# Optimization experiments

Measured on AMD Instinct MI355X. Metric: run time of the kernel, lower is better.

The kernel has to match this reference:

```python
import jax, jax.numpy as jnp
import numpy as np

B, T, V = 8, 1024, 2048

def setup_inputs() -> dict:
    key = jax.random.key(0)
    k1, k2, k3 = jax.random.split(key, 3)
    idx = jax.random.randint(k1, (B, T), 0, V)
    v_weight = jnp.zeros((T, 1), dtype=jnp.float32) + 0.02 * jax.random.normal(k2, (T, 1), dtype=jnp.float32)
    W = 0.01 * jnp.ones((V, V), dtype=jnp.float32) + 0.001 * jax.random.normal(k3, (V, V), dtype=jnp.float32)
    return {"idx": idx, "v_weight": v_weight, "W": W}

def reference(idx, v_weight, W):
    Tn = idx.shape[1]
    Vn = W.shape[0]
    e = jax.nn.one_hot(idx, Vn, dtype=jnp.float32)            # [B,T,V]
    pos = jnp.arange(Tn)
    rel = jnp.maximum(pos[:, None] - pos[None, :], 0)          # [T,T] clamped relative positions
    causal = pos[:, None] >= pos[None, :]                      # True where attention allowed
    # Layer 1: positional attention (shared across batch)
    a1 = v_weight[rel, 0]                                      # [T,T] gather from v embedding
    a1 = jnp.where(causal, a1, -jnp.inf)
    a1 = jax.nn.softmax(a1, axis=-1)
    layer_one = jnp.einsum('ts,bsv->btv', a1, e)               # [B,T,V]
    key_t = layer_one @ W.T                                    # Linear without bias: x @ W^T
    # Layer 2: content attention
    a2 = jnp.einsum('btv,bsv->bts', e, key_t)                  # [B,T,T]
    a2 = jnp.where(causal[None], a2, -jnp.inf)
    a2 = jax.nn.softmax(a2, axis=-1)
    logits = jnp.einsum('bts,bsv->btv', a2, e)                 # [B,T,V]
    return logits
```

## Files before the change

kernel.cpp:

```cpp
#include <hip/hip_runtime.h>
#include <hip/hip_bf16.h>
#include <math.h>

#define Bn 8
#define Tn 1024
#define Vn 2048

typedef __attribute__((ext_vector_type(8))) __bf16 bf16x8;
typedef __attribute__((ext_vector_type(4))) float floatx4;

#define GLDS(gp, lp) \
    __builtin_amdgcn_global_load_lds( \
        (const __attribute__((address_space(1))) void*)(gp), \
        (__attribute__((address_space(3))) void*)(lp), 16, 0, 0)

__global__ __launch_bounds__(256) void k_prep(const int* __restrict__ idx,
                                              const float* __restrict__ W,
                                              const float* __restrict__ vw,
                                              __hip_bfloat16* __restrict__ Abf,
                                              __hip_bfloat16* __restrict__ BT) {
    __shared__ float sbuf[Vn];
    int tid = threadIdx.x;
    if (blockIdx.y == Bn) {
        int s = blockIdx.x;
        int wave = tid >> 6, lane = tid & 63;
        float part = 0.0f;
#pragma unroll
        for (int i = 0; i < 4; ++i) {
            int d = tid + i * 256;
            if (d <= s) part += __expf(vw[d]);
        }
#pragma unroll
        for (int off = 32; off > 0; off >>= 1) part += __shfl_xor(part, off);
        if (lane == 0) sbuf[wave] = part;
        __syncthreads();
        float cinv = 1.0f / (sbuf[0] + sbuf[1] + sbuf[2] + sbuf[3]);
        int k0 = tid * 4;
        ushort u[4];
#pragma unroll
        for (int j = 0; j < 4; ++j) {
            int k = k0 + j;
            float v = (k <= s) ? __expf(vw[s - k]) * cinv : 0.0f;
            __hip_bfloat16 h = __float2bfloat16(v);
            u[j] = *reinterpret_cast<ushort*>(&h);
        }
        *reinterpret_cast<ushort4*>(&BT[(size_t)s * Tn + k0]) =
            make_ushort4(u[0], u[1], u[2], u[3]);
    } else {
        int b = blockIdx.y, t = blockIdx.x;
        int r = idx[b * Tn + t];
        const float* Wr = W + (size_t)r * Vn;
#pragma unroll
        for (int i = 0; i < 2; ++i) {
            int o = (tid + i * 256) * 4;
            *reinterpret_cast<float4*>(&sbuf[o]) = *reinterpret_cast<const float4*>(&Wr[o]);
        }
        int kmax = ((t >> 7) + 1) << 7;
        int k0 = tid * 4;
        int4 c4 = *reinterpret_cast<const int4*>(&idx[b * Tn + k0]);
        __syncthreads();
        if (k0 < kmax) {
            ushort u[4];
            __hip_bfloat16 h;
            h = __float2bfloat16(sbuf[c4.x]); u[0] = *reinterpret_cast<ushort*>(&h);
            h = __float2bfloat16(sbuf[c4.y]); u[1] = *reinterpret_cast<ushort*>(&h);
            h = __float2bfloat16(sbuf[c4.z]); u[2] = *reinterpret_cast<ushort*>(&h);
            h = __float2bfloat16(sbuf[c4.w]); u[3] = *reinterpret_cast<ushort*>(&h);
            *reinterpret_cast<ushort4*>(&Abf[((size_t)(b * Tn + t)) * Tn + k0]) =
                make_ushort4(u[0], u[1], u[2], u[3]);
        }
    }
}

#define TM 128
#define TN 128
#define NCHUNK 46

__device__ const signed char CH_MI[NCHUNK] = {7,7,6,7,5,6,7,4,5,6,7,3,4,5,6,7,
                                              6,7,2,3,4,5,6,7,
                                              5,6,7,1,2,3,4,5,6,7,
                                              4,5,6,7,0,1,2,3,4,5,6,7};
__device__ const signed char CH_NI[NCHUNK] = {7,7,6,6,5,5,5,4,4,4,4,3,3,3,3,3,
                                              6,6,2,2,2,2,2,2,
                                              5,5,5,1,1,1,1,1,1,1,
                                              4,4,4,4,0,0,0,0,0,0,0,0};
__device__ const signed char CH_K0[NCHUNK] = {0,8,0,0,0,0,0,0,0,0,0,0,0,0,0,0,
                                              8,8,0,0,0,0,0,0,
                                              8,8,8,0,0,0,0,0,0,0,
                                              8,8,8,8,0,0,0,0,0,0,0,0};
__device__ const signed char CH_K1[NCHUNK] = {8,16,8,8,8,8,8,8,8,8,8,8,8,8,8,8,
                                              14,14,6,6,6,6,6,6,
                                              12,12,12,4,4,4,4,4,4,4,
                                              10,10,10,10,2,2,2,2,2,2,2,2};
__device__ const signed char CH_P[NCHUNK]  = {0,1,0,0,0,0,0,0,0,0,0,0,0,0,0,0,
                                              1,1,0,0,0,0,0,0,
                                              1,1,1,0,0,0,0,0,0,0,
                                              1,1,1,1,0,0,0,0,0,0,0,0};

__global__ __launch_bounds__(256) void k_gemm(const __hip_bfloat16* __restrict__ A,
                                              const __hip_bfloat16* __restrict__ BT,
                                              float* __restrict__ part0,
                                              float* __restrict__ part1) {
    __shared__ __align__(16) __hip_bfloat16 As[16 * 512];
    __shared__ __align__(16) __hip_bfloat16 Bs[16 * 512];
    int b = blockIdx.x;
    int cidx = blockIdx.y;
    int mi = CH_MI[cidx], ni = CH_NI[cidx];
    int ki0 = CH_K0[cidx], ki1 = CH_K1[cidx];
    int m0 = mi * TM, n0 = ni * TN;
    int tid = threadIdx.x;
    int wave = tid >> 6, lane = tid & 63;
    int lr = lane & 15, lq = lane >> 4;
    int wmsub = (wave >> 1) * 4, wnsub = (wave & 1) * 4;

    const __hip_bfloat16* Ab = A + (size_t)b * Tn * Tn;

    const __hip_bfloat16* aS[4];
    const __hip_bfloat16* bS[4];
    __hip_bfloat16* aD[4];
    __hip_bfloat16* bD[4];
#pragma unroll
    for (int j = 0; j < 4; ++j) {
        int c = wave * 4 + j;
        int sub = c & 7, h = c >> 3;
        aS[j] = Ab + (size_t)(m0 + sub * 16 + lr) * Tn + h * 32 + lq * 8;
        bS[j] = BT + (size_t)(n0 + sub * 16 + lr) * Tn + h * 32 + lq * 8;
        aD[j] = &As[c * 512];
        bD[j] = &Bs[c * 512];
    }

    floatx4 acc[4][4];
#pragma unroll
    for (int i = 0; i < 4; ++i)
#pragma unroll
        for (int j = 0; j < 4; ++j) acc[i][j] = (floatx4){0.f, 0.f, 0.f, 0.f};

    for (int ki = ki0; ki < ki1; ++ki) {
        int ko = ki * 64;
#pragma unroll
        for (int j = 0; j < 4; ++j) {
            GLDS(aS[j] + ko, aD[j]);
            GLDS(bS[j] + ko, bD[j]);
        }
        __syncthreads();
        bf16x8 af[2][4], bfr[2][4];
#pragma unroll
        for (int h = 0; h < 2; ++h) {
#pragma unroll
            for (int m = 0; m < 4; ++m)
                af[h][m] = *reinterpret_cast<const bf16x8*>(
                    &As[(h * 8 + wmsub + m) * 512 + lane * 8]);
#pragma unroll
            for (int n = 0; n < 4; ++n)
                bfr[h][n] = *reinterpret_cast<const bf16x8*>(
                    &Bs[(h * 8 + wnsub + n) * 512 + lane * 8]);
        }
#pragma unroll
        for (int h = 0; h < 2; ++h)
#pragma unroll
            for (int m = 0; m < 4; ++m)
#pragma unroll
                for (int n = 0; n < 4; ++n)
                    acc[m][n] = __builtin_amdgcn_mfma_f32_16x16x32_bf16(
                        af[h][m], bfr[h][n], acc[m][n], 0, 0, 0);
        __syncthreads();
    }

    float* Cb = (CH_P[cidx] ? part1 : part0) + (size_t)b * Tn * Tn;
    int quad = lane >> 4;
#pragma unroll
    for (int m = 0; m < 4; ++m)
#pragma unroll
        for (int n = 0; n < 4; ++n)
#pragma unroll
            for (int r = 0; r < 4; ++r) {
                int row = m0 + wmsub * 16 + m * 16 + quad * 4 + r;
                int col = n0 + wnsub * 16 + n * 16 + lr;
                Cb[(size_t)row * Tn + col] = acc[m][n][r];
            }
}

__global__ __launch_bounds__(256) void k_softscat(const float* __restrict__ part0,
                                                  const float* __restrict__ part1,
                                                  const int* __restrict__ idx,
                                                  float* __restrict__ out) {
    __shared__ float sh[Vn];
    __shared__ float red[4];
    int t = blockIdx.x, b = blockIdx.y, tid = threadIdx.x;
    int wave = tid >> 6, lane = tid & 63;
#pragma unroll
    for (int i = 0; i < Vn / 256; ++i) sh[tid + i * 256] = 0.0f;

    size_t rowoff = ((size_t)b * Tn + t) * Tn;
    int s0 = tid * 4;
    float v[4] = {0.f, 0.f, 0.f, 0.f};
    if (s0 <= t) {
        float4 v4 = *reinterpret_cast<const float4*>(&part0[rowoff + s0]);
        v[0] = v4.x; v[1] = v4.y; v[2] = v4.z; v[3] = v4.w;
        if (s0 >= 512) {
            float4 w4 = *reinterpret_cast<const float4*>(&part1[rowoff + s0]);
            v[0] += w4.x; v[1] += w4.y; v[2] += w4.z; v[3] += w4.w;
        }
    }
    int4 c4 = *reinterpret_cast<const int4*>(&idx[b * Tn + s0]);
    float e[4];
    float lsum = 0.f;
#pragma unroll
    for (int j = 0; j < 4; ++j) {
        e[j] = (s0 + j <= t) ? __expf(v[j]) : 0.0f;
        lsum += e[j];
    }
#pragma unroll
    for (int off = 32; off > 0; off >>= 1) lsum += __shfl_xor(lsum, off);
    if (lane == 0) red[wave] = lsum;
    __syncthreads();
    float inv = 1.0f / (red[0] + red[1] + red[2] + red[3]);
    int c[4] = {c4.x, c4.y, c4.z, c4.w};
#pragma unroll
    for (int j = 0; j < 4; ++j)
        if (s0 + j <= t) atomicAdd(&sh[c[j]], e[j] * inv);
    __syncthreads();
    float* orow = out + ((size_t)b * Tn + t) * Vn;
#pragma unroll
    for (int i = 0; i < Vn / (256 * 4); ++i) {
        floatx4 val = *reinterpret_cast<const floatx4*>(&sh[(tid + i * 256) * 4]);
        __builtin_nontemporal_store(val,
            reinterpret_cast<floatx4*>(&orow[(tid + i * 256) * 4]));
    }
}

extern "C" void kernel_launch(void* const* d_in, const int* in_sizes, int n_in,
                              void* d_out, int out_size, void* d_ws, size_t ws_size,
                              hipStream_t stream) {
    const int* idx = (const int*)d_in[0];
    const float* vw = (const float*)d_in[1];
    const float* W = (const float*)d_in[2];
    float* out = (float*)d_out;
    char* ws = (char*)d_ws;

    __hip_bfloat16* BT = (__hip_bfloat16*)(ws);
    __hip_bfloat16* Abf = (__hip_bfloat16*)(ws + (2u << 20));
    float* part0 = (float*)(ws + (18u << 20));
    float* part1 = (float*)(ws + (52u << 20));

    k_prep<<<dim3(Tn, Bn + 1), 256, 0, stream>>>(idx, W, vw, Abf, BT);
    k_gemm<<<dim3(Bn, NCHUNK), 256, 0, stream>>>(Abf, BT, part0, part1);
    k_softscat<<<dim3(Tn, Bn), 256, 0, stream>>>(part0, part1, idx, out);
}
```

Before: 136.5 us.

## Double-buffer GEMM LDS tiles and stream W rows via global_load_lds

The GEMM main loop now uses two LDS buffers, issuing the next k-tile's direct-to-LDS loads before computing the current tile. Explicit vmcnt waits and raw barriers replace the syncthreads, so global latency can overlap MFMA work. The prep kernel also loads the gathered W row straight into LDS with global_load_lds and skips idx loads for columns past the causal limit. This doubles LDS use per GEMM block, which may reduce occupancy, and depends on hand-written waitcnt values being correct.

```diff
diff --git a/kernel.cpp b/kernel.cpp
--- a/kernel.cpp
+++ b/kernel.cpp
@@ -19,7 +19,7 @@
                                               const float* __restrict__ vw,
                                               __hip_bfloat16* __restrict__ Abf,
                                               __hip_bfloat16* __restrict__ BT) {
-    __shared__ float sbuf[Vn];
+    __shared__ __align__(16) float sbuf[Vn];
     int tid = threadIdx.x;
     if (blockIdx.y == Bn) {
         int s = blockIdx.x;
@@ -48,16 +48,17 @@
             make_ushort4(u[0], u[1], u[2], u[3]);
     } else {
         int b = blockIdx.y, t = blockIdx.x;
+        int wave = tid >> 6;
         int r = idx[b * Tn + t];
         const float* Wr = W + (size_t)r * Vn;
 #pragma unroll
         for (int i = 0; i < 2; ++i) {
-            int o = (tid + i * 256) * 4;
-            *reinterpret_cast<float4*>(&sbuf[o]) = *reinterpret_cast<const float4*>(&Wr[o]);
+            GLDS(Wr + i * 1024 + tid * 4, &sbuf[i * 1024 + wave * 256]);
         }
         int kmax = ((t >> 7) + 1) << 7;
         int k0 = tid * 4;
-        int4 c4 = *reinterpret_cast<const int4*>(&idx[b * Tn + k0]);
+        int4 c4 = make_int4(0, 0, 0, 0);
+        if (k0 < kmax) c4 = *reinterpret_cast<const int4*>(&idx[b * Tn + k0]);
         __syncthreads();
         if (k0 < kmax) {
             ushort u[4];
@@ -75,6 +76,7 @@
 #define TM 128
 #define TN 128
 #define NCHUNK 46
+#define BUFE (16 * 512)
 
 __device__ const signed char CH_MI[NCHUNK] = {7,7,6,7,5,6,7,4,5,6,7,3,4,5,6,7,
                                               6,7,2,3,4,5,6,7,
@@ -101,8 +103,8 @@
                                               const __hip_bfloat16* __restrict__ BT,
                                               float* __restrict__ part0,
                                               float* __restrict__ part1) {
-    __shared__ __align__(16) __hip_bfloat16 As[16 * 512];
-    __shared__ __align__(16) __hip_bfloat16 Bs[16 * 512];
+    __shared__ __align__(16) __hip_bfloat16 As[2 * BUFE];
+    __shared__ __align__(16) __hip_bfloat16 Bs[2 * BUFE];
     int b = blockIdx.x;
     int cidx = blockIdx.y;
     int mi = CH_MI[cidx], ni = CH_NI[cidx];
@@ -135,25 +137,42 @@
 #pragma unroll
         for (int j = 0; j < 4; ++j) acc[i][j] = (floatx4){0.f, 0.f, 0.f, 0.f};
 
+#pragma unroll
+    for (int j = 0; j < 4; ++j) {
+        GLDS(aS[j] + ki0 * 64, aD[j]);
+        GLDS(bS[j] + ki0 * 64, bD[j]);
+    }
+
     for (int ki = ki0; ki < ki1; ++ki) {
-        int ko = ki * 64;
-#pragma unroll
-        for (int j = 0; j < 4; ++j) {
-            GLDS(aS[j] + ko, aD[j]);
-            GLDS(bS[j] + ko, bD[j]);
-        }
-        __syncthreads();
+        int p = (ki - ki0) & 1;
+        if (ki + 1 < ki1) {
+            int ko = (ki + 1) * 64;
+            int off = (p ^ 1) * BUFE;
+#pragma unroll
+            for (int j = 0; j < 4; ++j) {
+                GLDS(aS[j] + ko, aD[j] + off);
+                GLDS(bS[j] + ko, bD[j] + off);
+            }
+            asm volatile("s_waitcnt vmcnt(8)" ::: "memory");
+        } else {
+            asm volatile("s_waitcnt vmcnt(0)" ::: "memory");
+        }
+        __builtin_amdgcn_s_barrier();
+        __builtin_amdgcn_sched_barrier(0);
+
+        const __hip_bfloat16* Asp = As + p * BUFE;
+        const __hip_bfloat16* Bsp = Bs + p * BUFE;
         bf16x8 af[2][4], bfr[2][4];
 #pragma unroll
         for (int h = 0; h < 2; ++h) {
 #pragma unroll
             for (int m = 0; m < 4; ++m)
                 af[h][m] = *reinterpret_cast<const bf16x8*>(
-                    &As[(h * 8 + wmsub + m) * 512 + lane * 8]);
+                    &Asp[(h * 8 + wmsub + m) * 512 + lane * 8]);
 #pragma unroll
             for (int n = 0; n < 4; ++n)
                 bfr[h][n] = *reinterpret_cast<const bf16x8*>(
-                    &Bs[(h * 8 + wnsub + n) * 512 + lane * 8]);
+                    &Bsp[(h * 8 + wnsub + n) * 512 + lane * 8]);
         }
 #pragma unroll
         for (int h = 0; h < 2; ++h)
@@ -163,7 +182,9 @@
                 for (int n = 0; n < 4; ++n)
                     acc[m][n] = __builtin_amdgcn_mfma_f32_16x16x32_bf16(
                         af[h][m], bfr[h][n], acc[m][n], 0, 0, 0);
-        __syncthreads();
+
+        __builtin_amdgcn_sched_barrier(0);
+        __builtin_amdgcn_s_barrier();
     }
 
     float* Cb = (CH_P[cidx] ? part1 : part0) + (size_t)b * Tn * Tn;
```

Result: no change. 134.1 us (-1.8%).
